# Kernel tuning notes

Measured on AMD Instinct MI355X. Metric: run time of the kernel, lower is better.

## Reference

```python
import jax, jax.numpy as jnp
import numpy as np


def setup_inputs() -> dict:
    key = jax.random.key(0)
    k1, k2, k3, k4, k5, k6 = jax.random.split(key, 6)
    B, N, D, H = 32, 4096, 256, 256
    return {
        "queries": jax.random.normal(k1, (B, N, D), dtype=jnp.float32),
        "keys": jax.random.normal(k2, (B, N, D), dtype=jnp.float32),
        "values": jax.random.normal(k3, (B, N, D), dtype=jnp.float32),
        "Wq": jax.random.normal(k4, (H, D), dtype=jnp.float32) * (1.0 / np.sqrt(D)),
        "Wk": jax.random.normal(k5, (H, D), dtype=jnp.float32) * (1.0 / np.sqrt(D)),
        "Wv": jax.random.normal(k6, (1, H), dtype=jnp.float32) * (1.0 / np.sqrt(H)),
    }


def reference(queries, keys, values, Wq, Wk, Wv):
    # Project queries and keys to hidden dim (torch Linear weight is [out, in])
    q = jnp.einsum('bnd,hd->bnh', queries, Wq)   # [B, N, H]
    k = jnp.einsum('bnd,hd->bnh', keys, Wk)      # [B, N, H]
    features = jnp.tanh(q + k)                   # [B, N, H]
    scores = jnp.einsum('bnh,oh->bno', features, Wv)  # [B, N, 1]
    alpha = jax.nn.softmax(scores, axis=1)       # softmax over N
    # dropout p=0 -> identity
    aggr_max = jnp.argmax(alpha, axis=1)         # [B, 1]
    out = jnp.sum(alpha * values, axis=1)        # [B, D]
    return (out, aggr_max)
```

## Files before the change

### kernel.cpp

```cpp
#include <hip/hip_runtime.h>

#define Bb 32
#define Nn 4096
#define Dd 256
#define Hh 256
#define NCH 32
#define CHUNK 128
#define NSTEPS 16

typedef __attribute__((ext_vector_type(8))) short bf16x8;
typedef __attribute__((ext_vector_type(4))) float f32x4;

__device__ __forceinline__ unsigned short bf16_rtn(float x) {
    unsigned int u = __float_as_uint(x);
    u += 0x7FFF + ((u >> 16) & 1);
    return (unsigned short)(u >> 16);
}
__device__ __forceinline__ float bf16_to_f(unsigned short b) {
    return __uint_as_float(((unsigned int)b) << 16);
}
__device__ __forceinline__ float fast_tanhf(float x) {
    float e = __expf(2.0f * x);
    return 1.0f - 2.0f / (e + 1.0f);
}

__device__ __forceinline__ void split8_store(short* hp, short* lp, f32x4 v0, f32x4 v1) {
    float xs[8] = {v0.x, v0.y, v0.z, v0.w, v1.x, v1.y, v1.z, v1.w};
    unsigned int hu[4], lu[4];
#pragma unroll
    for (int p = 0; p < 4; ++p) {
        unsigned int u0 = __float_as_uint(xs[2 * p]);
        unsigned int u1 = __float_as_uint(xs[2 * p + 1]);
        float r0 = xs[2 * p]     - __uint_as_float(u0 & 0xFFFF0000u);
        float r1 = xs[2 * p + 1] - __uint_as_float(u1 & 0xFFFF0000u);
        hu[p] = __builtin_amdgcn_perm(u1, u0, 0x07060302u);
        lu[p] = __builtin_amdgcn_perm(__float_as_uint(r1), __float_as_uint(r0), 0x07060302u);
    }
    *(uint4*)hp = make_uint4(hu[0], hu[1], hu[2], hu[3]);
    *(uint4*)lp = make_uint4(lu[0], lu[1], lu[2], lu[3]);
}

__global__ __launch_bounds__(256) void prep_w_kernel(
    const float* __restrict__ Wq, const float* __restrict__ Wk,
    short* __restrict__ Wh, short* __restrict__ Wl)
{
    const int g = blockIdx.x * 256 + threadIdx.x;
    const int s = g >> 10;
    const int j = (g >> 6) & 15;
    const int l = g & 63;
    const int n = j * 16 + (l & 15);
    const int k = s * 32 + (l >> 4) * 8;
    const float* src = (k < 256) ? (Wq + n * 256 + k) : (Wk + n * 256 + (k - 256));
    const f32x4 v0 = *(const f32x4*)src;
    const f32x4 v1 = *(const f32x4*)(src + 4);
    float xs[8] = {v0.x, v0.y, v0.z, v0.w, v1.x, v1.y, v1.z, v1.w};
    bf16x8 h8, l8;
#pragma unroll
    for (int e = 0; e < 8; ++e) {
        unsigned short hb = bf16_rtn(xs[e]);
        float rem = xs[e] - bf16_to_f(hb);
        h8[e] = (short)hb;
        l8[e] = (short)bf16_rtn(rem);
    }
    *(bf16x8*)&Wh[(size_t)g * 8] = h8;
    *(bf16x8*)&Wl[(size_t)g * 8] = l8;
}

__global__ __launch_bounds__(256, 2) void scores_mfma_kernel(
    const float* __restrict__ Q, const float* __restrict__ Kmat,
    const short* __restrict__ Wh, const short* __restrict__ Wl,
    const float* __restrict__ Wv, float* __restrict__ scores)
{
    __shared__ short Ah[3][4096];
    __shared__ short Al[3][4096];
    __shared__ float red[4][128];

    const int tid = threadIdx.x;
    const int lane = tid & 63;
    const int wave = tid >> 6;
    const size_t row0 = (size_t)blockIdx.x * 128;

    f32x4 acc[8][4];
#pragma unroll
    for (int m = 0; m < 8; ++m)
#pragma unroll
        for (int n = 0; n < 4; ++n) acc[m][n] = (f32x4){0.f, 0.f, 0.f, 0.f};

    float wv[4];
#pragma unroll
    for (int n = 0; n < 4; ++n) wv[n] = Wv[wave * 64 + n * 16 + (lane & 15)];

    const int r_s0 = ((tid >> 6) << 4) + (tid & 15);
    const int r_s1 = r_s0 + 64;
    const int k_s0 = ((tid >> 4) & 3) * 8;

    f32x4 pA0, pA1, pA2, pA3;
    f32x4 qA0, qA1, qA2, qA3;
    bf16x8 bh[4], bl[4];

    auto issue_aP = [&](int s) {
        if (s >= NSTEPS) return;
        const float* Asrc = (s < 8) ? Q : Kmat;
        const int kb = (s & 7) * 32 + k_s0;
        const float* p0 = Asrc + (row0 + r_s0) * Dd + kb;
        const float* p1 = Asrc + (row0 + r_s1) * Dd + kb;
        pA0 = *(const f32x4*)p0; pA1 = *(const f32x4*)(p0 + 4);
        pA2 = *(const f32x4*)p1; pA3 = *(const f32x4*)(p1 + 4);
    };
    auto issue_aQ = [&](int s) {
        if (s >= NSTEPS) return;
        const float* Asrc = (s < 8) ? Q : Kmat;
        const int kb = (s & 7) * 32 + k_s0;
        const float* p0 = Asrc + (row0 + r_s0) * Dd + kb;
        const float* p1 = Asrc + (row0 + r_s1) * Dd + kb;
        qA0 = *(const f32x4*)p0; qA1 = *(const f32x4*)(p0 + 4);
        qA2 = *(const f32x4*)p1; qA3 = *(const f32x4*)(p1 + 4);
    };
    auto issue_b = [&](int s) {
#pragma unroll
        for (int n = 0; n < 4; ++n) {
            const size_t bo = ((size_t)(s * 16 + wave * 4 + n) * 64 + lane) * 8;
            bh[n] = *(const bf16x8*)(Wh + bo);
            bl[n] = *(const bf16x8*)(Wl + bo);
        }
    };
    auto splitP = [&](int buf) {
        split8_store(&Ah[buf][tid * 8], &Al[buf][tid * 8], pA0, pA1);
        split8_store(&Ah[buf][(tid + 256) * 8], &Al[buf][(tid + 256) * 8], pA2, pA3);
    };
    auto splitQ = [&](int buf) {
        split8_store(&Ah[buf][tid * 8], &Al[buf][tid * 8], qA0, qA1);
        split8_store(&Ah[buf][(tid + 256) * 8], &Al[buf][(tid + 256) * 8], qA2, qA3);
    };
    auto cluster = [&](int rb) {
        const short* ahb = &Ah[rb][0];
        const short* alb = &Al[rb][0];
        __builtin_amdgcn_s_setprio(1);
#pragma unroll
        for (int m = 0; m < 8; ++m) {
            const bf16x8 ahm = *(const bf16x8*)&ahb[(m * 64 + lane) * 8];
            const bf16x8 alm = *(const bf16x8*)&alb[(m * 64 + lane) * 8];
#pragma unroll
            for (int n = 0; n < 4; ++n) {
                acc[m][n] = __builtin_amdgcn_mfma_f32_16x16x32_bf16(ahm, bh[n], acc[m][n], 0, 0, 0);
                acc[m][n] = __builtin_amdgcn_mfma_f32_16x16x32_bf16(alm, bh[n], acc[m][n], 0, 0, 0);
                acc[m][n] = __builtin_amdgcn_mfma_f32_16x16x32_bf16(ahm, bl[n], acc[m][n], 0, 0, 0);
            }
        }
        __builtin_amdgcn_s_setprio(0);
    };

    issue_aP(0);
    issue_aQ(1);
    splitP(0);
    __syncthreads();

    int rb = 0;
    for (int s2 = 0; s2 < NSTEPS / 2; ++s2) {
        const int s = 2 * s2;
        issue_b(s);
        issue_aP(s + 2);
        cluster(rb);
        if (s + 1 < NSTEPS) splitQ(rb == 2 ? 0 : rb + 1);
        __syncthreads();
        issue_b(s + 1);
        issue_aQ(s + 3);
        cluster(rb == 2 ? 0 : rb + 1);
        if (s + 2 < NSTEPS) splitP(rb >= 1 ? rb - 1 : rb + 2);
        __syncthreads();
        rb = (rb >= 1) ? rb - 1 : rb + 2;
    }

    const int q = lane >> 4;
    float rp[8][4];
#pragma unroll
    for (int m = 0; m < 8; ++m)
#pragma unroll
        for (int r = 0; r < 4; ++r) {
            float v = 0.f;
#pragma unroll
            for (int n = 0; n < 4; ++n)
                v += wv[n] * fast_tanhf(acc[m][n][r]);
            rp[m][r] = v;
        }
#pragma unroll
    for (int mask = 1; mask <= 8; mask <<= 1)
#pragma unroll
        for (int m = 0; m < 8; ++m)
#pragma unroll
            for (int r = 0; r < 4; ++r)
                rp[m][r] += __shfl_xor(rp[m][r], mask, 64);

    if ((lane & 15) == 0) {
#pragma unroll
        for (int m = 0; m < 8; ++m)
#pragma unroll
            for (int r = 0; r < 4; ++r)
                red[wave][m * 16 + q * 4 + r] = rp[m][r];
    }
    __syncthreads();
    if (tid < 128)
        scores[row0 + tid] = (red[0][tid] + red[1][tid]) + (red[2][tid] + red[3][tid]);
}

__global__ __launch_bounds__(256) void softmax_reduce_kernel(
    const float* __restrict__ scores, float* __restrict__ mbuf,
    float* __restrict__ zbuf, float* __restrict__ out)
{
    __shared__ float sv[256];
    __shared__ int si[256];
    const int b = blockIdx.x;
    const int tid = threadIdx.x;
    const float* sc = scores + (size_t)b * Nn;

    float best = -1e30f; int bi = 0;
    for (int j = 0; j < Nn / 256; ++j) {
        const int n = tid + j * 256;
        const float v = sc[n];
        if (v > best) { best = v; bi = n; }
    }
    sv[tid] = best; si[tid] = bi;
    __syncthreads();
    for (int off = 128; off > 0; off >>= 1) {
        if (tid < off) {
            const float v2 = sv[tid + off]; const int i2 = si[tid + off];
            if (v2 > sv[tid] || (v2 == sv[tid] && i2 < si[tid])) { sv[tid] = v2; si[tid] = i2; }
        }
        __syncthreads();
    }
    const float m = sv[0];
    const int amax = si[0];
    __syncthreads();

    float ssum = 0.f;
    for (int j = 0; j < Nn / 256; ++j) ssum += __expf(sc[tid + j * 256] - m);
    sv[tid] = ssum;
    __syncthreads();
    for (int off = 128; off > 0; off >>= 1) {
        if (tid < off) sv[tid] += sv[tid + off];
        __syncthreads();
    }
    if (tid == 0) {
        mbuf[b] = m;
        zbuf[b] = sv[0];
        out[(size_t)Bb * Dd + b] = (float)amax;
    }
}

__global__ __launch_bounds__(256) void partial_kernel(
    const float* __restrict__ V, const float* __restrict__ scores,
    const float* __restrict__ mbuf, float* __restrict__ part)
{
    __shared__ float e[CHUNK];
    const int c = blockIdx.x;
    const int b = blockIdx.y;
    const int tid = threadIdx.x;
    const float m = mbuf[b];
    if (tid < CHUNK)
        e[tid] = __expf(scores[(size_t)b * Nn + (size_t)c * CHUNK + tid] - m);
    __syncthreads();

    const float* vp = V + ((size_t)b * Nn + (size_t)c * CHUNK) * Dd + tid;
    float a0 = 0.f, a1 = 0.f, a2 = 0.f, a3 = 0.f;
    for (int n = 0; n < CHUNK; n += 4) {
        a0 = fmaf(e[n + 0], vp[(size_t)(n + 0) * Dd], a0);
        a1 = fmaf(e[n + 1], vp[(size_t)(n + 1) * Dd], a1);
        a2 = fmaf(e[n + 2], vp[(size_t)(n + 2) * Dd], a2);
        a3 = fmaf(e[n + 3], vp[(size_t)(n + 3) * Dd], a3);
    }
    part[((size_t)b * NCH + c) * Dd + tid] = ((a0 + a1) + (a2 + a3));
}

__global__ __launch_bounds__(256) void finalize_kernel(
    const float* __restrict__ part, const float* __restrict__ zbuf,
    float* __restrict__ out)
{
    const int b = blockIdx.x;
    const int tid = threadIdx.x;
    float s = 0.f;
#pragma unroll
    for (int c = 0; c < NCH; ++c) s += part[((size_t)b * NCH + c) * Dd + tid];
    out[(size_t)b * Dd + tid] = s / zbuf[b];
}

extern "C" void kernel_launch(void* const* d_in, const int* in_sizes, int n_in,
                              void* d_out, int out_size, void* d_ws, size_t ws_size,
                              hipStream_t stream) {
    const float* Q  = (const float*)d_in[0];
    const float* K  = (const float*)d_in[1];
    const float* V  = (const float*)d_in[2];
    const float* Wq = (const float*)d_in[3];
    const float* Wk = (const float*)d_in[4];
    const float* Wv = (const float*)d_in[5];
    float* out = (float*)d_out;

    char* wsb = (char*)d_ws;
    short* Wh     = (short*)(wsb);
    short* Wl     = (short*)(wsb + 262144);
    float* scores = (float*)(wsb + 524288);
    float* mbuf   = (float*)(wsb + 1048576);
    float* zbuf   = (float*)(wsb + 1048576 + 128);
    float* part   = (float*)(wsb + 1048576 + 256);

    prep_w_kernel<<<dim3(64), dim3(256), 0, stream>>>(Wq, Wk, Wh, Wl);
    scores_mfma_kernel<<<dim3((Bb * Nn) / 128), dim3(256), 0, stream>>>(Q, K, Wh, Wl, Wv, scores);
    softmax_reduce_kernel<<<dim3(Bb), dim3(256), 0, stream>>>(scores, mbuf, zbuf, out);
    partial_kernel<<<dim3(NCH, Bb), dim3(256), 0, stream>>>(V, scores, mbuf, part);
    finalize_kernel<<<dim3(Bb), dim3(256), 0, stream>>>(part, zbuf, out);
}
```

Measured before the change: 132.5 us.

## Restructure GEMM main loop with B-prefetch and lighter barriers

Reorders the software pipeline so that the weight (B) fragments for the next step are fetched after the current MFMA cluster instead of right before it, and peels the final iterations so the bounds checks in the A-load lambdas can be dropped. It also replaces __syncthreads with a barrier that waits only on LDS counters, so outstanding global loads can stay in flight across the barrier. The aim is to hide global load latency behind compute and sync. In exchange it keeps more registers live and leans on the manual waitcnt being correct.

```diff
diff --git a/kernel.cpp b/kernel.cpp
--- a/kernel.cpp
+++ b/kernel.cpp
@@ -99,7 +99,6 @@
     bf16x8 bh[4], bl[4];
 
     auto issue_aP = [&](int s) {
-        if (s >= NSTEPS) return;
         const float* Asrc = (s < 8) ? Q : Kmat;
         const int kb = (s & 7) * 32 + k_s0;
         const float* p0 = Asrc + (row0 + r_s0) * Dd + kb;
@@ -108,7 +107,6 @@
         pA2 = *(const f32x4*)p1; pA3 = *(const f32x4*)(p1 + 4);
     };
     auto issue_aQ = [&](int s) {
-        if (s >= NSTEPS) return;
         const float* Asrc = (s < 8) ? Q : Kmat;
         const int kb = (s & 7) * 32 + k_s0;
         const float* p0 = Asrc + (row0 + r_s0) * Dd + kb;
@@ -149,27 +147,40 @@
         }
         __builtin_amdgcn_s_setprio(0);
     };
+    auto barrier_nv = [&]() {
+        asm volatile("s_waitcnt lgkmcnt(0)" ::: "memory");
+        __builtin_amdgcn_s_barrier();
+        asm volatile("" ::: "memory");
+    };
 
     issue_aP(0);
     issue_aQ(1);
+    issue_b(0);
     splitP(0);
-    __syncthreads();
+    barrier_nv();
 
     int rb = 0;
-    for (int s2 = 0; s2 < NSTEPS / 2; ++s2) {
+    for (int s2 = 0; s2 < 7; ++s2) {
         const int s = 2 * s2;
-        issue_b(s);
+        const int rb1 = (rb == 2) ? 0 : rb + 1;
+        const int rb2 = (rb1 == 2) ? 0 : rb1 + 1;
+        cluster(rb);
+        splitQ(rb1);
+        issue_b(s + 1);
         issue_aP(s + 2);
-        cluster(rb);
-        if (s + 1 < NSTEPS) splitQ(rb == 2 ? 0 : rb + 1);
-        __syncthreads();
-        issue_b(s + 1);
+        barrier_nv();
+        cluster(rb1);
+        splitP(rb2);
+        issue_b(s + 2);
         issue_aQ(s + 3);
-        cluster(rb == 2 ? 0 : rb + 1);
-        if (s + 2 < NSTEPS) splitP(rb >= 1 ? rb - 1 : rb + 2);
-        __syncthreads();
-        rb = (rb >= 1) ? rb - 1 : rb + 2;
-    }
+        barrier_nv();
+        rb = rb2;
+    }
+    cluster(2);
+    splitQ(0);
+    issue_b(15);
+    barrier_nv();
+    cluster(0);
 
     const int q = lane >> 4;
     float rp[8][4];
```

Measured after the change: 135.3 us. 1.02x slower.

## Use single-pass fp16 MFMA for scores with fp64 argmax tie refinement

Applied to the files above, without the earlier changes.

Replaces the three-pass bf16 hi/lo split GEMM with a single fp16 MFMA pass, which cuts MFMA work to a third, halves LDS traffic and drops the weight lo-part loads. The software pipeline is restructured with double B register sets and a peeled final step. To keep argmax exact despite the lower precision, the softmax kernel gathers near-max candidates within a threshold and recomputes their scores in double precision. The added candidate recompute adds serial work per batch, and fp16 may lose accuracy on the softmax-weighted sum.

```diff
diff --git a/kernel.cpp b/kernel.cpp
--- a/kernel.cpp
+++ b/kernel.cpp
@@ -8,41 +8,26 @@
 #define CHUNK 128
 #define NSTEPS 16
 
-typedef __attribute__((ext_vector_type(8))) short bf16x8;
+typedef __attribute__((ext_vector_type(8))) _Float16 half8;
 typedef __attribute__((ext_vector_type(4))) float f32x4;
 
-__device__ __forceinline__ unsigned short bf16_rtn(float x) {
-    unsigned int u = __float_as_uint(x);
-    u += 0x7FFF + ((u >> 16) & 1);
-    return (unsigned short)(u >> 16);
-}
-__device__ __forceinline__ float bf16_to_f(unsigned short b) {
-    return __uint_as_float(((unsigned int)b) << 16);
-}
 __device__ __forceinline__ float fast_tanhf(float x) {
     float e = __expf(2.0f * x);
     return 1.0f - 2.0f / (e + 1.0f);
 }
 
-__device__ __forceinline__ void split8_store(short* hp, short* lp, f32x4 v0, f32x4 v1) {
-    float xs[8] = {v0.x, v0.y, v0.z, v0.w, v1.x, v1.y, v1.z, v1.w};
-    unsigned int hu[4], lu[4];
-#pragma unroll
-    for (int p = 0; p < 4; ++p) {
-        unsigned int u0 = __float_as_uint(xs[2 * p]);
-        unsigned int u1 = __float_as_uint(xs[2 * p + 1]);
-        float r0 = xs[2 * p]     - __uint_as_float(u0 & 0xFFFF0000u);
-        float r1 = xs[2 * p + 1] - __uint_as_float(u1 & 0xFFFF0000u);
-        hu[p] = __builtin_amdgcn_perm(u1, u0, 0x07060302u);
-        lu[p] = __builtin_amdgcn_perm(__float_as_uint(r1), __float_as_uint(r0), 0x07060302u);
-    }
-    *(uint4*)hp = make_uint4(hu[0], hu[1], hu[2], hu[3]);
-    *(uint4*)lp = make_uint4(lu[0], lu[1], lu[2], lu[3]);
+__device__ __forceinline__ half8 cvt8(f32x4 v0, f32x4 v1) {
+    half8 h;
+    h[0] = (_Float16)v0.x; h[1] = (_Float16)v0.y;
+    h[2] = (_Float16)v0.z; h[3] = (_Float16)v0.w;
+    h[4] = (_Float16)v1.x; h[5] = (_Float16)v1.y;
+    h[6] = (_Float16)v1.z; h[7] = (_Float16)v1.w;
+    return h;
 }
 
 __global__ __launch_bounds__(256) void prep_w_kernel(
     const float* __restrict__ Wq, const float* __restrict__ Wk,
-    short* __restrict__ Wh, short* __restrict__ Wl)
+    _Float16* __restrict__ Wf)
 {
     const int g = blockIdx.x * 256 + threadIdx.x;
     const int s = g >> 10;
@@ -53,26 +38,15 @@
     const float* src = (k < 256) ? (Wq + n * 256 + k) : (Wk + n * 256 + (k - 256));
     const f32x4 v0 = *(const f32x4*)src;
     const f32x4 v1 = *(const f32x4*)(src + 4);
-    float xs[8] = {v0.x, v0.y, v0.z, v0.w, v1.x, v1.y, v1.z, v1.w};
-    bf16x8 h8, l8;
-#pragma unroll
-    for (int e = 0; e < 8; ++e) {
-        unsigned short hb = bf16_rtn(xs[e]);
-        float rem = xs[e] - bf16_to_f(hb);
-        h8[e] = (short)hb;
-        l8[e] = (short)bf16_rtn(rem);
-    }
-    *(bf16x8*)&Wh[(size_t)g * 8] = h8;
-    *(bf16x8*)&Wl[(size_t)g * 8] = l8;
+    *(half8*)&Wf[(size_t)g * 8] = cvt8(v0, v1);
 }
 
 __global__ __launch_bounds__(256, 2) void scores_mfma_kernel(
     const float* __restrict__ Q, const float* __restrict__ Kmat,
-    const short* __restrict__ Wh, const short* __restrict__ Wl,
+    const _Float16* __restrict__ Wf,
     const float* __restrict__ Wv, float* __restrict__ scores)
 {
-    __shared__ short Ah[3][4096];
-    __shared__ short Al[3][4096];
+    __shared__ _Float16 Ahf[3][4096];
     __shared__ float red[4][128];
 
     const int tid = threadIdx.x;
@@ -96,10 +70,9 @@
 
     f32x4 pA0, pA1, pA2, pA3;
     f32x4 qA0, qA1, qA2, qA3;
-    bf16x8 bh[4], bl[4];
+    half8 BA[4], BB[4];
 
     auto issue_aP = [&](int s) {
-        if (s >= NSTEPS) return;
         const float* Asrc = (s < 8) ? Q : Kmat;
         const int kb = (s & 7) * 32 + k_s0;
         const float* p0 = Asrc + (row0 + r_s0) * Dd + kb;
@@ -108,7 +81,6 @@
         pA2 = *(const f32x4*)p1; pA3 = *(const f32x4*)(p1 + 4);
     };
     auto issue_aQ = [&](int s) {
-        if (s >= NSTEPS) return;
         const float* Asrc = (s < 8) ? Q : Kmat;
         const int kb = (s & 7) * 32 + k_s0;
         const float* p0 = Asrc + (row0 + r_s0) * Dd + kb;
@@ -116,60 +88,75 @@
         qA0 = *(const f32x4*)p0; qA1 = *(const f32x4*)(p0 + 4);
         qA2 = *(const f32x4*)p1; qA3 = *(const f32x4*)(p1 + 4);
     };
-    auto issue_b = [&](int s) {
-#pragma unroll
-        for (int n = 0; n < 4; ++n) {
-            const size_t bo = ((size_t)(s * 16 + wave * 4 + n) * 64 + lane) * 8;
-            bh[n] = *(const bf16x8*)(Wh + bo);
-            bl[n] = *(const bf16x8*)(Wl + bo);
-        }
-    };
-    auto splitP = [&](int buf) {
-        split8_store(&Ah[buf][tid * 8], &Al[buf][tid * 8], pA0, pA1);
-        split8_store(&Ah[buf][(tid + 256) * 8], &Al[buf][(tid + 256) * 8], pA2, pA3);
-    };
-    auto splitQ = [&](int buf) {
-        split8_store(&Ah[buf][tid * 8], &Al[buf][tid * 8], qA0, qA1);
-        split8_store(&Ah[buf][(tid + 256) * 8], &Al[buf][(tid + 256) * 8], qA2, qA3);
-    };
-    auto cluster = [&](int rb) {
-        const short* ahb = &Ah[rb][0];
-        const short* alb = &Al[rb][0];
+    auto issue_bA = [&](int s) {
+#pragma unroll
+        for (int n = 0; n < 4; ++n)
+            BA[n] = *(const half8*)(Wf + ((size_t)(s * 16 + wave * 4 + n) * 64 + lane) * 8);
+    };
+    auto issue_bB = [&](int s) {
+#pragma unroll
+        for (int n = 0; n < 4; ++n)
+            BB[n] = *(const half8*)(Wf + ((size_t)(s * 16 + wave * 4 + n) * 64 + lane) * 8);
+    };
+    auto storeP = [&](int buf) {
+        *(half8*)&Ahf[buf][tid * 8] = cvt8(pA0, pA1);
+        *(half8*)&Ahf[buf][(tid + 256) * 8] = cvt8(pA2, pA3);
+    };
+    auto storeQ = [&](int buf) {
+        *(half8*)&Ahf[buf][tid * 8] = cvt8(qA0, qA1);
+        *(half8*)&Ahf[buf][(tid + 256) * 8] = cvt8(qA2, qA3);
+    };
+    auto clusterA = [&](int rb) {
         __builtin_amdgcn_s_setprio(1);
 #pragma unroll
         for (int m = 0; m < 8; ++m) {
-            const bf16x8 ahm = *(const bf16x8*)&ahb[(m * 64 + lane) * 8];
-            const bf16x8 alm = *(const bf16x8*)&alb[(m * 64 + lane) * 8];
-#pragma unroll
-            for (int n = 0; n < 4; ++n) {
-                acc[m][n] = __builtin_amdgcn_mfma_f32_16x16x32_bf16(ahm, bh[n], acc[m][n], 0, 0, 0);
-                acc[m][n] = __builtin_amdgcn_mfma_f32_16x16x32_bf16(alm, bh[n], acc[m][n], 0, 0, 0);
-                acc[m][n] = __builtin_amdgcn_mfma_f32_16x16x32_bf16(ahm, bl[n], acc[m][n], 0, 0, 0);
-            }
+            const half8 ahm = *(const half8*)&Ahf[rb][(m * 64 + lane) * 8];
+#pragma unroll
+            for (int n = 0; n < 4; ++n)
+                acc[m][n] = __builtin_amdgcn_mfma_f32_16x16x32_f16(ahm, BA[n], acc[m][n], 0, 0, 0);
+        }
+        __builtin_amdgcn_s_setprio(0);
+    };
+    auto clusterB = [&](int rb) {
+        __builtin_amdgcn_s_setprio(1);
+#pragma unroll
+        for (int m = 0; m < 8; ++m) {
+            const half8 ahm = *(const half8*)&Ahf[rb][(m * 64 + lane) * 8];
+#pragma unroll
+            for (int n = 0; n < 4; ++n)
+                acc[m][n] = __builtin_amdgcn_mfma_f32_16x16x32_f16(ahm, BB[n], acc[m][n], 0, 0, 0);
         }
         __builtin_amdgcn_s_setprio(0);
     };
 
     issue_aP(0);
     issue_aQ(1);
-    splitP(0);
+    issue_bA(0);
+    storeP(0);
     __syncthreads();
 
     int rb = 0;
-    for (int s2 = 0; s2 < NSTEPS / 2; ++s2) {
+    for (int s2 = 0; s2 < 7; ++s2) {
         const int s = 2 * s2;
-        issue_b(s);
+        const int rb1 = (rb == 2) ? 0 : rb + 1;
+        const int rb2 = (rb1 == 2) ? 0 : rb1 + 1;
+        issue_bB(s + 1);
         issue_aP(s + 2);
-        cluster(rb);
-        if (s + 1 < NSTEPS) splitQ(rb == 2 ? 0 : rb + 1);
+        clusterA(rb);
+        storeQ(rb1);
         __syncthreads();
-        issue_b(s + 1);
+        issue_bA(s + 2);
         issue_aQ(s + 3);
-        cluster(rb == 2 ? 0 : rb + 1);
-        if (s + 2 < NSTEPS) splitP(rb >= 1 ? rb - 1 : rb + 2);
+        clusterB(rb1);
+        storeP(rb2);
         __syncthreads();
-        rb = (rb >= 1) ? rb - 1 : rb + 2;
-    }
+        rb = rb2;
+    }
+    issue_bB(15);
+    clusterA(2);
+    storeQ(0);
+    __syncthreads();
+    clusterB(0);
 
     const int q = lane >> 4;
     float rp[8][4];
@@ -203,12 +190,19 @@
         scores[row0 + tid] = (red[0][tid] + red[1][tid]) + (red[2][tid] + red[3][tid]);
 }
 
+#define MAXC 64
 __global__ __launch_bounds__(256) void softmax_reduce_kernel(
-    const float* __restrict__ scores, float* __restrict__ mbuf,
-    float* __restrict__ zbuf, float* __restrict__ out)
+    const float* __restrict__ scores,
+    const float* __restrict__ Qg, const float* __restrict__ Kg,
+    const float* __restrict__ Wq, const float* __restrict__ Wk,
+    const float* __restrict__ Wv,
+    float* __restrict__ mbuf, float* __restrict__ zbuf, float* __restrict__ out)
 {
     __shared__ float sv[256];
     __shared__ int si[256];
+    __shared__ double dred[256];
+    __shared__ int cand[MAXC];
+    __shared__ int cnt;
     const int b = blockIdx.x;
     const int tid = threadIdx.x;
     const float* sc = scores + (size_t)b * Nn;
@@ -229,7 +223,7 @@
         __syncthreads();
     }
     const float m = sv[0];
-    const int amax = si[0];
+    int amax = si[0];
     __syncthreads();
 
     float ssum = 0.f;
@@ -240,9 +234,48 @@
         if (tid < off) sv[tid] += sv[tid + off];
         __syncthreads();
     }
+    const float Z = sv[0];
+    __syncthreads();
+
+    if (tid == 0) cnt = 0;
+    __syncthreads();
+    const float tau = 0.008f;
+    for (int j = 0; j < Nn / 256; ++j) {
+        const int n = tid + j * 256;
+        if (sc[n] >= m - tau) {
+            const int p = atomicAdd(&cnt, 1);
+            if (p < MAXC) cand[p] = n;
+        }
+    }
+    __syncthreads();
+    const int ncand = (cnt < MAXC) ? cnt : MAXC;
+    if (ncand > 1) {
+        double bestv = -1e300; int besti = 0x7fffffff;
+        for (int c = 0; c < ncand; ++c) {
+            const int n = cand[c];
+            const float* qr = Qg + ((size_t)b * Nn + n) * Dd;
+            const float* kr = Kg + ((size_t)b * Nn + n) * Dd;
+            const float* wqr = Wq + tid * Dd;
+            const float* wkr = Wk + tid * Dd;
+            double accd = 0.0;
+            for (int k2 = 0; k2 < Dd; ++k2)
+                accd += (double)qr[k2] * (double)wqr[k2] + (double)kr[k2] * (double)wkr[k2];
+            dred[tid] = (double)Wv[tid] * tanh(accd);
+            __syncthreads();
+            for (int off = 128; off > 0; off >>= 1) {
+                if (tid < off) dred[tid] += dred[tid + off];
+                __syncthreads();
+            }
+            const double s_c = dred[0];
+            __syncthreads();
+            if (s_c > bestv || (s_c == bestv && n < besti)) { bestv = s_c; besti = n; }
+        }
+        amax = besti;
+    }
+
     if (tid == 0) {
         mbuf[b] = m;
-        zbuf[b] = sv[0];
+        zbuf[b] = Z;
         out[(size_t)Bb * Dd + b] = (float)amax;
     }
 }
@@ -295,16 +328,15 @@
     float* out = (float*)d_out;
 
     char* wsb = (char*)d_ws;
-    short* Wh     = (short*)(wsb);
-    short* Wl     = (short*)(wsb + 262144);
-    float* scores = (float*)(wsb + 524288);
-    float* mbuf   = (float*)(wsb + 1048576);
-    float* zbuf   = (float*)(wsb + 1048576 + 128);
-    float* part   = (float*)(wsb + 1048576 + 256);
-
-    prep_w_kernel<<<dim3(64), dim3(256), 0, stream>>>(Wq, Wk, Wh, Wl);
-    scores_mfma_kernel<<<dim3((Bb * Nn) / 128), dim3(256), 0, stream>>>(Q, K, Wh, Wl, Wv, scores);
-    softmax_reduce_kernel<<<dim3(Bb), dim3(256), 0, stream>>>(scores, mbuf, zbuf, out);
+    _Float16* Wf  = (_Float16*)(wsb);
+    float* scores = (float*)(wsb + 262144);
+    float* mbuf   = (float*)(wsb + 786432);
+    float* zbuf   = (float*)(wsb + 786432 + 128);
+    float* part   = (float*)(wsb + 786432 + 256);
+
+    prep_w_kernel<<<dim3(64), dim3(256), 0, stream>>>(Wq, Wk, Wf);
+    scores_mfma_kernel<<<dim3((Bb * Nn) / 128), dim3(256), 0, stream>>>(Q, K, Wf, Wv, scores);
+    softmax_reduce_kernel<<<dim3(Bb), dim3(256), 0, stream>>>(scores, Q, K, Wq, Wk, Wv, mbuf, zbuf, out);
     partial_kernel<<<dim3(NCH, Bb), dim3(256), 0, stream>>>(V, scores, mbuf, part);
     finalize_kernel<<<dim3(Bb), dim3(256), 0, stream>>>(part, zbuf, out);
 }
```

After: 123.3 us. 1.07x faster.
